# Kernel tuning notes

Hardware: AMD Instinct MI355X
Metric: run time of the kernel (lower is better)

The kernel has to match this reference:

```python
import jax, jax.numpy as jnp
import numpy as np

# Body-part joint index groups (NTU-25 layout), as in the torch module
TORSO = np.array([0, 1, 2, 3, 20])
LEFT_HAND = np.array([8, 9, 10, 11, 23, 24])
LEFT_LEG = np.array([16, 17, 18, 19])
RIGHT_HAND = np.array([4, 5, 6, 7, 21, 22])
RIGHT_LEG = np.array([12, 13, 14, 15])
GROUPS = [TORSO, LEFT_HAND, LEFT_LEG, RIGHT_HAND, RIGHT_LEG]

N, C, T, V = 64, 256, 64, 25
HID = C // 16


def setup_inputs() -> dict:
    key = jax.random.key(0)
    k = jax.random.split(key, 5)
    x = jax.random.normal(k[0], (N, C, T, V), dtype=jnp.float32)
    # 5 branch MLPs (1x1 convs == linear over channels), stacked on leading axis f
    W1s = jax.random.normal(k[1], (5, HID, C), dtype=jnp.float32) * (1.0 / np.sqrt(C))
    b1s = jax.random.normal(k[2], (5, HID), dtype=jnp.float32) * 0.01
    W2s = jax.random.normal(k[3], (5, C, HID), dtype=jnp.float32) * (1.0 / np.sqrt(HID))
    b2s = jax.random.normal(k[4], (5, C), dtype=jnp.float32) * 0.01
    return {"x": x, "W1s": W1s, "b1s": b1s, "W2s": W2s, "b2s": b2s}


def _branch_mlp(p, W1s, b1s, W2s, b2s):
    # p: [N, C] pooled features; apply all 5 branch MLPs at once -> [N, 5, C]
    h = jax.nn.relu(jnp.einsum("nc,fhc->nfh", p, W1s) + b1s[None])  # [N,5,HID]
    return jnp.einsum("nfh,fch->nfc", h, W2s) + b2s[None]  # [N,5,C]


def reference(x, W1s, b1s, W2s, b2s):
    torso = x[:, :, :, TORSO]  # [N,C,T,5]
    avg = jnp.mean(torso, axis=(2, 3))  # [N,C] (AdaptiveAvgPool2d(1))
    mx = jnp.max(torso, axis=(2, 3))  # [N,C] (AdaptiveMaxPool2d(1))
    gates = jax.nn.sigmoid(_branch_mlp(avg, W1s, b1s, W2s, b2s)
                           + _branch_mlp(mx, W1s, b1s, W2s, b2s))  # [N,5,C]
    parts = [x[:, :, :, idx] * gates[:, i][:, :, None, None]
             for i, idx in enumerate(GROUPS)]
    return jnp.concatenate(parts, axis=3)  # [N,C,T,25]
```

## Files before the change

### kernel.cpp

```cpp
#include <hip/hip_runtime.h>
#include <math.h>

#define NB   64
#define CC   256
#define TT   64
#define VV   25
#define HID  16
#define NG   5
#define ROWF 1600
#define ROWF4 400
#define PAIRS 4

#define TORSO_MASK 0x10000Fu

__constant__ int PERM_LUT[25] = {
    0|(0<<8), 1|(0<<8), 2|(0<<8), 3|(0<<8), 20|(0<<8),
    8|(1<<8), 9|(1<<8), 10|(1<<8), 11|(1<<8), 23|(1<<8), 24|(1<<8),
    16|(2<<8), 17|(2<<8), 18|(2<<8), 19|(2<<8),
    4|(3<<8), 5|(3<<8), 6|(3<<8), 7|(3<<8), 21|(3<<8), 22|(3<<8),
    12|(4<<8), 13|(4<<8), 14|(4<<8), 15|(4<<8)
};

__global__ void pool_kernel(const float4* __restrict__ x4,
                            float* __restrict__ avg_out,
                            float* __restrict__ max_out) {
    const int wave = threadIdx.x >> 6;
    const int lane = threadIdx.x & 63;
    const int pair = blockIdx.x * 4 + wave;
    const int base4 = pair * ROWF4;

    float s = 0.0f;
    float m = -3.4e38f;
    for (int i = lane; i < ROWF4; i += 64) {
        float4 v = x4[base4 + i];
        const int e = 4 * i;
        int j = e % 25;
        float vals[4] = {v.x, v.y, v.z, v.w};
        #pragma unroll
        for (int k = 0; k < 4; ++k) {
            int jj = j + k;
            if (jj >= 25) jj -= 25;
            if ((TORSO_MASK >> jj) & 1u) {
                s += vals[k];
                m = fmaxf(m, vals[k]);
            }
        }
    }
    #pragma unroll
    for (int off = 32; off >= 1; off >>= 1) {
        s += __shfl_xor(s, off, 64);
        m = fmaxf(m, __shfl_xor(m, off, 64));
    }
    if (lane == 0) {
        avg_out[pair] = s * (1.0f / (TT * 5));
        max_out[pair] = m;
    }
}

__global__ void gates_kernel(const float* __restrict__ avg_in,
                             const float* __restrict__ max_in,
                             const float* __restrict__ W1s,
                             const float* __restrict__ b1s,
                             const float* __restrict__ W2s,
                             const float* __restrict__ b2s,
                             float* __restrict__ gates) {
    __shared__ float4 sAvg[CC / 4];
    __shared__ float4 sMax[CC / 4];
    __shared__ float sHA[NG * HID];
    __shared__ float sHM[NG * HID];

    const int n = blockIdx.x;
    const int tid = threadIdx.x;

    if (tid < 64)       sAvg[tid]      = reinterpret_cast<const float4*>(avg_in + n * CC)[tid];
    else if (tid < 128) sMax[tid - 64] = reinterpret_cast<const float4*>(max_in + n * CC)[tid - 64];
    __syncthreads();

    if (tid < 2 * NG * HID) {
        const int type = tid / (NG * HID);
        const int rem  = tid % (NG * HID);
        const float4* p = type ? sMax : sAvg;
        const float4* w = reinterpret_cast<const float4*>(W1s + rem * CC);
        float h = b1s[rem];
        #pragma unroll 8
        for (int c4 = 0; c4 < CC / 4; ++c4) {
            float4 a = w[c4], b = p[c4];
            h += a.x * b.x + a.y * b.y + a.z * b.z + a.w * b.w;
        }
        h = fmaxf(h, 0.0f);
        if (type) sHM[rem] = h; else sHA[rem] = h;
    }
    __syncthreads();

    const int c = tid;
    #pragma unroll
    for (int f = 0; f < NG; ++f) {
        const float4* w2 = reinterpret_cast<const float4*>(W2s + (f * CC + c) * HID);
        float g = 2.0f * b2s[f * CC + c];
        #pragma unroll
        for (int j4 = 0; j4 < HID / 4; ++j4) {
            float4 w = w2[j4];
            const int jb = f * HID + j4 * 4;
            g += w.x * (sHA[jb + 0] + sHM[jb + 0]);
            g += w.y * (sHA[jb + 1] + sHM[jb + 1]);
            g += w.z * (sHA[jb + 2] + sHM[jb + 2]);
            g += w.w * (sHA[jb + 3] + sHM[jb + 3]);
        }
        gates[(n * NG + f) * CC + c] = 1.0f / (1.0f + expf(-g));
    }
}

__global__ void apply_kernel(const float4* __restrict__ x4,
                             const float* __restrict__ gates,
                             float4* __restrict__ out4) {
    __shared__ float lds[PAIRS * ROWF];
    __shared__ float sg[PAIRS * NG];
    __shared__ int sLut[VV];

    const int tid = threadIdx.x;
    const int nc0 = blockIdx.x * PAIRS;
    const int base4 = nc0 * ROWF4;

    #pragma unroll
    for (int i = tid; i < PAIRS * ROWF4; i += 256) {
        reinterpret_cast<float4*>(lds)[i] = x4[base4 + i];
    }
    if (tid < PAIRS * NG) {
        const int q = tid / NG, f = tid % NG;
        const int nc = nc0 + q;
        sg[tid] = gates[((nc >> 8) * NG + f) * CC + (nc & (CC - 1))];
    }
    if (tid < VV) sLut[tid] = PERM_LUT[tid];
    __syncthreads();

    #pragma unroll
    for (int i = tid; i < PAIRS * ROWF4; i += 256) {
        const int q = i / ROWF4;
        const int e0 = 4 * (i - q * ROWF4);
        int row = e0 / 25;
        int p   = e0 - row * 25;
        const float* lrow = lds + q * ROWF;
        const float* gq   = sg + q * NG;
        float r[4];
        #pragma unroll
        for (int k = 0; k < 4; ++k) {
            const int lut = sLut[p];
            r[k] = lrow[row * 25 + (lut & 0xFF)] * gq[lut >> 8];
            ++p;
            if (p >= 25) { p = 0; ++row; }
        }
        out4[base4 + i] = make_float4(r[0], r[1], r[2], r[3]);
    }
}

extern "C" void kernel_launch(void* const* d_in, const int* in_sizes, int n_in,
                              void* d_out, int out_size, void* d_ws, size_t ws_size,
                              hipStream_t stream) {
    const float* x   = (const float*)d_in[0];
    const float* W1s = (const float*)d_in[1];
    const float* b1s = (const float*)d_in[2];
    const float* W2s = (const float*)d_in[3];
    const float* b2s = (const float*)d_in[4];

    float* avg   = (float*)d_ws;
    float* mx    = avg + NB * CC;
    float* gates = mx + NB * CC;

    pool_kernel<<<(NB * CC) / 4, 256, 0, stream>>>(
        (const float4*)x, avg, mx);

    gates_kernel<<<NB, CC, 0, stream>>>(avg, mx, W1s, b1s, W2s, b2s, gates);

    apply_kernel<<<(NB * CC) / PAIRS, 256, 0, stream>>>(
        (const float4*)x, gates, (float4*)d_out);
}
```

Before: 219.5 us.

## Use nontemporal output stores, smaller apply tiles, branchless torso masking in pool

The apply kernel now handles two (n,c) rows per block instead of four, which doubles the block count and halves LDS use per block. Its output writes become nontemporal vector stores so the large result stream bypasses cache retention. The pool kernel replaces its per-element modulo and branch with a precomputed 50-bit double mask and select-based accumulation. Together these aim to cut memory-side overhead in a bandwidth-bound pipeline, at the cost of more blocks, each with its own setup work.

```diff
diff --git a/kernel.cpp b/kernel.cpp
--- a/kernel.cpp
+++ b/kernel.cpp
@@ -9,11 +9,13 @@
 #define NG   5
 #define ROWF 1600
 #define ROWF4 400
-#define PAIRS 4
+#define PAIRS 2
 
 #define TORSO_MASK 0x10000Fu
 
-__constant__ int PERM_LUT[25] = {
+typedef float fx4 __attribute__((ext_vector_type(4)));
+
+__constant__ int PERM_LUT[VV] = {
     0|(0<<8), 1|(0<<8), 2|(0<<8), 3|(0<<8), 20|(0<<8),
     8|(1<<8), 9|(1<<8), 10|(1<<8), 11|(1<<8), 23|(1<<8), 24|(1<<8),
     16|(2<<8), 17|(2<<8), 18|(2<<8), 19|(2<<8),
@@ -29,22 +31,23 @@
     const int pair = blockIdx.x * 4 + wave;
     const int base4 = pair * ROWF4;
 
+    const unsigned long long M2 = (unsigned long long)TORSO_MASK
+                                | ((unsigned long long)TORSO_MASK << 25);
+    const float NEG = -3.4e38f;
     float s = 0.0f;
-    float m = -3.4e38f;
+    float m = NEG;
     for (int i = lane; i < ROWF4; i += 64) {
         float4 v = x4[base4 + i];
-        const int e = 4 * i;
-        int j = e % 25;
-        float vals[4] = {v.x, v.y, v.z, v.w};
-        #pragma unroll
-        for (int k = 0; k < 4; ++k) {
-            int jj = j + k;
-            if (jj >= 25) jj -= 25;
-            if ((TORSO_MASK >> jj) & 1u) {
-                s += vals[k];
-                m = fmaxf(m, vals[k]);
-            }
-        }
+        const int j = (4 * i) % 25;
+        const unsigned bits = (unsigned)((M2 >> j) & 0xFULL);
+        s += (bits & 1u) ? v.x : 0.0f;
+        s += (bits & 2u) ? v.y : 0.0f;
+        s += (bits & 4u) ? v.z : 0.0f;
+        s += (bits & 8u) ? v.w : 0.0f;
+        m = fmaxf(m, (bits & 1u) ? v.x : NEG);
+        m = fmaxf(m, (bits & 2u) ? v.y : NEG);
+        m = fmaxf(m, (bits & 4u) ? v.z : NEG);
+        m = fmaxf(m, (bits & 8u) ? v.w : NEG);
     }
     #pragma unroll
     for (int off = 32; off >= 1; off >>= 1) {
@@ -110,9 +113,10 @@
     }
 }
 
-__global__ void apply_kernel(const float4* __restrict__ x4,
-                             const float* __restrict__ gates,
-                             float4* __restrict__ out4) {
+__global__ __launch_bounds__(256)
+void apply_kernel(const float4* __restrict__ x4,
+                  const float* __restrict__ gates,
+                  fx4* __restrict__ out4) {
     __shared__ float lds[PAIRS * ROWF];
     __shared__ float sg[PAIRS * NG];
     __shared__ int sLut[VV];
@@ -141,7 +145,7 @@
         int p   = e0 - row * 25;
         const float* lrow = lds + q * ROWF;
         const float* gq   = sg + q * NG;
-        float r[4];
+        fx4 r;
         #pragma unroll
         for (int k = 0; k < 4; ++k) {
             const int lut = sLut[p];
@@ -149,7 +153,7 @@
             ++p;
             if (p >= 25) { p = 0; ++row; }
         }
-        out4[base4 + i] = make_float4(r[0], r[1], r[2], r[3]);
+        __builtin_nontemporal_store(r, &out4[base4 + i]);
     }
 }
 
@@ -172,5 +176,5 @@
     gates_kernel<<<NB, CC, 0, stream>>>(avg, mx, W1s, b1s, W2s, b2s, gates);
 
     apply_kernel<<<(NB * CC) / PAIRS, 256, 0, stream>>>(
-        (const float4*)x, gates, (float4*)d_out);
+        (const float4*)x, gates, (fx4*)d_out);
 }
```

Result: no change. 217.8 us (median of 2 runs) (-0.8%).
